# Kernel tuning notes

Hardware: AMD Instinct MI355X
Metric: run time of the kernel (lower is better)

## Reference

```python
import jax, jax.numpy as jnp
import numpy as np

B, T, EMB, H = 8, 1024, 128, 8


def setup_inputs() -> dict:
    key = jax.random.key(0)
    ks = jax.random.split(key, 7)
    s = 0.02
    return {
        "x": jax.random.normal(ks[0], (B, T, EMB), dtype=jnp.float32),
        "mask": jax.random.randint(ks[1], (1, T, T), 0, 2, dtype=jnp.int32),
        "Wk": (jax.random.normal(ks[2], (EMB * H, EMB), dtype=jnp.float32) * s),
        "Wq": (jax.random.normal(ks[3], (EMB * H, EMB), dtype=jnp.float32) * s),
        "Wv": (jax.random.normal(ks[4], (EMB * H, EMB), dtype=jnp.float32) * s),
        "Wu": (jax.random.normal(ks[5], (EMB, EMB * H), dtype=jnp.float32) * s),
        "bu": (jax.random.normal(ks[6], (EMB,), dtype=jnp.float32) * s),
    }


def reference(x, mask, Wk, Wq, Wv, Wu, bu):
    b, t, e = x.shape  # e == emb; per-head dim also == emb in this module
    h = Wk.shape[0] // e
    # projections: (b,t,e) @ (e, h*e) -> (b,t,h,e) -> (b,h,t,e)
    q = (x @ Wq.T).reshape(b, t, h, e).transpose(0, 2, 1, 3)
    k = (x @ Wk.T).reshape(b, t, h, e).transpose(0, 2, 1, 3)
    v = (x @ Wv.T).reshape(b, t, h, e).transpose(0, 2, 1, 3)
    scale = e ** 0.25  # torch scales q and k each by e**(1/4)
    dot = jnp.einsum('bhqe,bhke->bhqk', q / scale, k / scale)
    # causal mask: strictly-upper triangle (offset=1) set to -inf FIRST
    causal = jnp.triu(jnp.ones((t, t), dtype=bool), k=1)
    dot = jnp.where(causal, -jnp.inf, dot)
    # padding mask: where mask==0 set to -1e9 (overwrites -inf where overlapping)
    dot = jnp.where(mask[:, None] == 0, jnp.float32(-1e9), dot)
    attn = jax.nn.softmax(dot, axis=-1)
    out = jnp.einsum('bhqk,bhke->bhqe', attn, v)
    out = out.transpose(0, 2, 1, 3).reshape(b, t, h * e)
    return out @ Wu.T + bu
```

## Files before the change

kernel.cpp:

```cpp
#include <hip/hip_runtime.h>

#define Bn 8
#define Hn 8
#define Tn 1024
#define Dn 128

typedef __attribute__((ext_vector_type(8))) short bf16x8;
typedef __attribute__((ext_vector_type(4))) float f32x4;

typedef __attribute__((address_space(3))) unsigned int lds_as_t;
typedef __attribute__((address_space(1))) const unsigned int glb_as_t;

static __device__ __forceinline__ void gload_lds16(const unsigned short* g, unsigned short* l) {
    __builtin_amdgcn_global_load_lds((glb_as_t*)g, (lds_as_t*)l, 16, 0, 0);
}

static __device__ __forceinline__ unsigned short f2bf(float f) {
    union { float f; unsigned int u; } v; v.f = f;
    unsigned int u = v.u;
    return (unsigned short)((u + 0x7FFFu + ((u >> 16) & 1u)) >> 16);
}

__global__ __launch_bounds__(256) void prep_kernel(
    const float* __restrict__ x,  const float* __restrict__ Wq,
    const float* __restrict__ Wk, const float* __restrict__ Wv,
    const float* __restrict__ Wu, const int* __restrict__ mask,
    unsigned short* __restrict__ xb,  unsigned short* __restrict__ wqB,
    unsigned short* __restrict__ wkB, unsigned short* __restrict__ wvB,
    unsigned short* __restrict__ wuB, unsigned long long* __restrict__ bits)
{
    const int blk = blockIdx.x;
    const int tid = threadIdx.x;

    if (blk < 1408) {
        const float* in; unsigned short* out; int i4;
        if (blk < 1024)      { in = x;  out = xb;  i4 = blk * 256 + tid; }
        else if (blk < 1152) { in = Wq; out = wqB; i4 = (blk - 1024) * 256 + tid; }
        else if (blk < 1280) { in = Wk; out = wkB; i4 = (blk - 1152) * 256 + tid; }
        else                 { in = Wv; out = wvB; i4 = (blk - 1280) * 256 + tid; }
        float4 f = ((const float4*)in)[i4];
        ushort4 o;
        o.x = f2bf(f.x); o.y = f2bf(f.y); o.z = f2bf(f.z); o.w = f2bf(f.w);
        int base = i4 * 4;
        int row = base >> 7, col = base & 127;
        int scol = (((col >> 3) ^ (row & 15)) << 3) | (col & 7);
        *(ushort4*)(out + row * 128 + scol) = o;
    } else if (blk < 1536) {
        int i4 = (blk - 1408) * 256 + tid;
        float4 f = ((const float4*)Wu)[i4];
        ushort4 o;
        o.x = f2bf(f.x); o.y = f2bf(f.y); o.z = f2bf(f.z); o.w = f2bf(f.w);
        ((ushort4*)wuB)[i4] = o;
    } else {
        int wid  = (blk - 1536) * 4 + (tid >> 6);
        int lane = tid & 63;
#pragma unroll
        for (int i = 0; i < 4; i++) {
            int widx = wid * 4 + i;
            int row = widx >> 4, kt = widx & 15;
            int v = mask[row * Tn + kt * 64 + lane];
            unsigned long long b = __ballot(v != 0);
            if (lane == 0) bits[widx] = b;
        }
    }
}

__global__ __launch_bounds__(256, 2) void qkv_kernel(
    const unsigned short* __restrict__ xb,
    const unsigned short* __restrict__ wqB,
    const unsigned short* __restrict__ wkB,
    const unsigned short* __restrict__ wvB,
    unsigned short* __restrict__ Q,
    unsigned short* __restrict__ K,
    unsigned short* __restrict__ Vt)
{
    const int bx = blockIdx.x, by = blockIdx.y;
    const int wave = threadIdx.x >> 6;
    const int lane = threadIdx.x & 63;
    const int l16  = lane & 15;
    const int quad = lane >> 4;
    const int wm = wave & 1, wn = wave >> 1;

    __shared__ __align__(16) unsigned short As[128 * 128];
    __shared__ __align__(16) unsigned short Bs[128 * 128];

    const int which = by >> 3;
    const unsigned short* wsel = (which == 0) ? wqB : (which == 1) ? wkB : wvB;
    const unsigned short* Ag = xb + (size_t)bx * 128 * 128;
    const unsigned short* Bg = wsel + (size_t)(by & 7) * 128 * 128;

#pragma unroll
    for (int i = 0; i < 8; i++) {
        int base = (wave * 8 + i) * 512;
        gload_lds16(Ag + base + lane * 8, &As[base]);
        gload_lds16(Bg + base + lane * 8, &Bs[base]);
    }
    __syncthreads();

    bf16x8 a[4][4];
#pragma unroll
    for (int mt = 0; mt < 4; mt++) {
        int row = wm * 64 + mt * 16 + l16;
#pragma unroll
        for (int ks = 0; ks < 4; ks++)
            a[mt][ks] = *(const bf16x8*)(&As[row * 128 + (((ks * 4 + quad) ^ (row & 15)) << 3)]);
    }

    f32x4 acc[4][4];
#pragma unroll
    for (int nt = 0; nt < 4; nt++) {
        int row = wn * 64 + nt * 16 + l16;
        bf16x8 b4[4];
#pragma unroll
        for (int ks = 0; ks < 4; ks++)
            b4[ks] = *(const bf16x8*)(&Bs[row * 128 + (((ks * 4 + quad) ^ (row & 15)) << 3)]);
#pragma unroll
        for (int mt = 0; mt < 4; mt++) {
            f32x4 c = {0.f, 0.f, 0.f, 0.f};
#pragma unroll
            for (int ks = 0; ks < 4; ks++)
                c = __builtin_amdgcn_mfma_f32_16x16x32_bf16(a[mt][ks], b4[ks], c, 0, 0, 0);
            acc[mt][nt] = c;
        }
    }

    const int h_ = by & 7;
#pragma unroll
    for (int mt = 0; mt < 4; mt++) {
        int m_base = bx * 128 + wm * 64 + mt * 16 + quad * 4;
        int b_ = m_base >> 10;
        int t0 = m_base & 1023;
#pragma unroll
        for (int nt = 0; nt < 4; nt++) {
            int ncol = wn * 64 + nt * 16 + l16;
            if (which == 2) {
                int kt_ = t0 >> 6, tc0 = t0 & 63;
                int e_ = ncol;
                size_t off = ((((size_t)(b_ * Hn + h_) * 16 + kt_) * 128 + e_) << 6)
                           + ((((tc0 >> 3) ^ (e_ & 7)) << 3) | (tc0 & 7));
                ushort4 v4;
                v4.x = f2bf(acc[mt][nt][0]); v4.y = f2bf(acc[mt][nt][1]);
                v4.z = f2bf(acc[mt][nt][2]); v4.w = f2bf(acc[mt][nt][3]);
                *(ushort4*)(Vt + off) = v4;
            } else {
#pragma unroll
                for (int r = 0; r < 4; r++) {
                    int t_ = t0 + r;
                    unsigned short v = f2bf(acc[mt][nt][r]);
                    size_t rowoff = ((size_t)((b_ * Hn + h_) * Tn + t_)) * Dn;
                    if (which == 0) {
                        Q[rowoff + ncol] = v;
                    } else {
                        int nc = ((((ncol >> 3) ^ (t_ & 15)) << 3) | (ncol & 7));
                        K[rowoff + nc] = v;
                    }
                }
            }
        }
    }
}

__global__ __launch_bounds__(256, 2) void attn_kernel(
    const unsigned short* __restrict__ Q,
    const unsigned short* __restrict__ K,
    const unsigned short* __restrict__ Vt,
    const unsigned long long* __restrict__ mbits,
    unsigned short* __restrict__ AO)
{
    const int qt   = 15 - ((blockIdx.x + blockIdx.y) & 15);
    const int bh   = blockIdx.y;
    const int wave = threadIdx.x >> 6;
    const int lane = threadIdx.x & 63;
    const int l16  = lane & 15;
    const int quad = lane >> 4;

    __shared__ __align__(16) unsigned short kbuf[2][64 * 128];
    __shared__ __align__(16) unsigned short vbuf[2][128 * 64];
    __shared__ __align__(16) unsigned short pbuf[4][16][72];

    const unsigned short* Qb = Q  + (size_t)bh * Tn * Dn;
    const unsigned short* Kb = K  + (size_t)bh * Tn * Dn;
    const unsigned short* Vb = Vt + (size_t)bh * (16 * 128 * 64);

    const int q0 = qt * 64 + wave * 16;
    const int qrow = q0 + quad * 4;
    const unsigned long long* mrow = mbits + (size_t)qrow * 16;

    bf16x8 qf[4];
#pragma unroll
    for (int ks = 0; ks < 4; ks++)
        qf[ks] = *(const bf16x8*)(Qb + (size_t)(q0 + l16) * Dn + ks * 32 + quad * 8);

    bf16x8 ones;
#pragma unroll
    for (int j = 0; j < 8; j++) ones[j] = (short)0x3F80;

    f32x4 o[8];
#pragma unroll
    for (int et = 0; et < 8; et++) o[et] = (f32x4){0.f, 0.f, 0.f, 0.f};
    f32x4 lacc = {0.f, 0.f, 0.f, 0.f};

    const float SL = 0.12752041570284543f;

#pragma unroll
    for (int i = 0; i < 4; i++) {
        int base = (wave * 4 + i) * 512;
        gload_lds16(Kb + base + lane * 8, &kbuf[0][base]);
        gload_lds16(Vb + base + lane * 8, &vbuf[0][base]);
    }

    for (int kt = 0; kt <= qt; kt++) {
        const int cur = kt & 1;
        __syncthreads();

        if (kt < qt) {
            const unsigned short* Kg = Kb + (kt + 1) * (64 * 128);
            const unsigned short* Vg = Vb + (kt + 1) * (128 * 64);
#pragma unroll
            for (int i = 0; i < 4; i++) {
                int base = (wave * 4 + i) * 512;
                gload_lds16(Kg + base + lane * 8, &kbuf[cur ^ 1][base]);
                gload_lds16(Vg + base + lane * 8, &vbuf[cur ^ 1][base]);
            }
        }

        unsigned long long mw[4];
#pragma unroll
        for (int r = 0; r < 4; r++) mw[r] = mrow[r * 16 + kt];

        f32x4 s[4];
#pragma unroll
        for (int nt = 0; nt < 4; nt++) {
            bf16x8 b4[4];
#pragma unroll
            for (int ks = 0; ks < 4; ks++)
                b4[ks] = *(const bf16x8*)(&kbuf[cur][(nt * 16 + l16) * 128 + (((ks * 4 + quad) ^ l16) << 3)]);
            f32x4 c = {0.f, 0.f, 0.f, 0.f};
#pragma unroll
            for (int ks = 0; ks < 4; ks++)
                c = __builtin_amdgcn_mfma_f32_16x16x32_bf16(qf[ks], b4[ks], c, 0, 0, 0);
            s[nt] = c;
        }

        const int kc0 = kt * 64;
#pragma unroll
        for (int nt = 0; nt < 4; nt++) {
            int bi = nt * 16 + l16;
            int key = kc0 + bi;
#pragma unroll
            for (int r = 0; r < 4; r++) {
                bool live = ((mw[r] >> bi) & 1ULL) && !(kt == qt && key > qrow + r);
                float p = live ? __builtin_amdgcn_exp2f(s[nt][r] * SL) : 0.f;
                pbuf[wave][quad * 4 + r][bi] = f2bf(p);
            }
        }

        bf16x8 pf[2];
#pragma unroll
        for (int k2 = 0; k2 < 2; k2++)
            pf[k2] = *(const bf16x8*)(&pbuf[wave][l16][k2 * 32 + quad * 8]);

#pragma unroll
        for (int k2 = 0; k2 < 2; k2++)
            lacc = __builtin_amdgcn_mfma_f32_16x16x32_bf16(pf[k2], ones, lacc, 0, 0, 0);
#pragma unroll
        for (int et = 0; et < 8; et++) {
            f32x4 c = o[et];
#pragma unroll
            for (int k2 = 0; k2 < 2; k2++) {
                bf16x8 b = *(const bf16x8*)(&vbuf[cur][(et * 16 + l16) * 64 + (((k2 * 4 + quad) ^ (l16 & 7)) << 3)]);
                c = __builtin_amdgcn_mfma_f32_16x16x32_bf16(pf[k2], b, c, 0, 0, 0);
            }
            o[et] = c;
        }
    }

    {
        bool deg = (lacc[0] == 0.f) | (lacc[1] == 0.f) | (lacc[2] == 0.f) | (lacc[3] == 0.f);
        if (__ballot(deg) != 0ULL) {
            unsigned short dsel[4];
#pragma unroll
            for (int r = 0; r < 4; r++) dsel[r] = (lacc[r] == 0.f) ? (unsigned short)0x3F80 : (unsigned short)0;
            for (int kt = 0; kt < 16; kt++) {
                unsigned long long mw[4];
#pragma unroll
                for (int r = 0; r < 4; r++) mw[r] = mrow[r * 16 + kt];
#pragma unroll
                for (int nt = 0; nt < 4; nt++) {
                    int bi = nt * 16 + l16;
#pragma unroll
                    for (int r = 0; r < 4; r++)
                        pbuf[wave][quad * 4 + r][bi] = ((mw[r] >> bi) & 1ULL) ? (unsigned short)0 : dsel[r];
                }
                bf16x8 pf[2];
#pragma unroll
                for (int k2 = 0; k2 < 2; k2++)
                    pf[k2] = *(const bf16x8*)(&pbuf[wave][l16][k2 * 32 + quad * 8]);
#pragma unroll
                for (int k2 = 0; k2 < 2; k2++)
                    lacc = __builtin_amdgcn_mfma_f32_16x16x32_bf16(pf[k2], ones, lacc, 0, 0, 0);
#pragma unroll
                for (int et = 0; et < 8; et++) {
                    f32x4 c = o[et];
#pragma unroll
                    for (int k2 = 0; k2 < 2; k2++) {
                        const unsigned short* vg = Vb + kt * (128 * 64)
                            + (et * 16 + l16) * 64 + (((k2 * 4 + quad) ^ (l16 & 7)) << 3);
                        bf16x8 b = *(const bf16x8*)vg;
                        c = __builtin_amdgcn_mfma_f32_16x16x32_bf16(pf[k2], b, c, 0, 0, 0);
                    }
                    o[et] = c;
                }
            }
        }
    }

    const int b_ = bh >> 3, h_ = bh & 7;
#pragma unroll
    for (int r = 0; r < 4; r++) {
        float inv = 1.f / lacc[r];
        int q = qrow + r;
        size_t rowoff = (size_t)(b_ * Tn + q) * (Hn * Dn) + h_ * Dn;
#pragma unroll
        for (int et = 0; et < 8; et++)
            AO[rowoff + et * 16 + l16] = f2bf(o[et][r] * inv);
    }
}

__global__ void zero_kernel(float4* __restrict__ p, int n4) {
    int i = blockIdx.x * blockDim.x + threadIdx.x;
    if (i < n4) p[i] = (float4){0.f, 0.f, 0.f, 0.f};
}

__global__ __launch_bounds__(256) void outproj_kernel(
    const unsigned short* __restrict__ AO,
    const unsigned short* __restrict__ wuB,
    const float* __restrict__ bu,
    float* __restrict__ out)
{
    const int wave = threadIdx.x >> 6;
    const int lane = threadIdx.x & 63;
    const int l16  = lane & 15;
    const int quad = lane >> 4;
    const int m0 = blockIdx.x * 64 + wave * 16;
    const int ks0 = blockIdx.y * 16;

    f32x4 acc[8];
#pragma unroll
    for (int nt = 0; nt < 8; nt++) acc[nt] = (f32x4){0.f, 0.f, 0.f, 0.f};

    for (int g = 0; g < 4; g++) {
        int kk = ks0 + g * 4;
        bf16x8 a4[4];
#pragma unroll
        for (int j = 0; j < 4; j++)
            a4[j] = *(const bf16x8*)(AO + (size_t)(m0 + l16) * 1024 + (kk + j) * 32 + quad * 8);
#pragma unroll
        for (int nt = 0; nt < 8; nt++) {
            bf16x8 b4[4];
#pragma unroll
            for (int j = 0; j < 4; j++)
                b4[j] = *(const bf16x8*)(wuB + (size_t)(nt * 16 + l16) * 1024 + (kk + j) * 32 + quad * 8);
#pragma unroll
            for (int j = 0; j < 4; j++)
                acc[nt] = __builtin_amdgcn_mfma_f32_16x16x32_bf16(a4[j], b4[j], acc[nt], 0, 0, 0);
        }
    }

#pragma unroll
    for (int nt = 0; nt < 8; nt++) {
        int n = nt * 16 + l16;
        float bias = (blockIdx.y == 0) ? bu[n] : 0.f;
#pragma unroll
        for (int r = 0; r < 4; r++) {
            int m = m0 + quad * 4 + r;
            atomicAdd(&out[(size_t)m * Dn + n], acc[nt][r] + bias);
        }
    }
}

extern "C" void kernel_launch(void* const* d_in, const int* in_sizes, int n_in,
                              void* d_out, int out_size, void* d_ws, size_t ws_size,
                              hipStream_t stream) {
    const float* x   = (const float*)d_in[0];
    const int* mask  = (const int*)d_in[1];
    const float* Wk  = (const float*)d_in[2];
    const float* Wq  = (const float*)d_in[3];
    const float* Wv  = (const float*)d_in[4];
    const float* Wu  = (const float*)d_in[5];
    const float* bu  = (const float*)d_in[6];
    float* out = (float*)d_out;

    char* ws = (char*)d_ws;
    unsigned short* xb  = (unsigned short*)ws; ws += (size_t)8192 * 128 * 2;
    unsigned short* wqB = (unsigned short*)ws; ws += (size_t)1024 * 128 * 2;
    unsigned short* wkB = (unsigned short*)ws; ws += (size_t)1024 * 128 * 2;
    unsigned short* wvB = (unsigned short*)ws; ws += (size_t)1024 * 128 * 2;
    unsigned short* wuB = (unsigned short*)ws; ws += (size_t)128 * 1024 * 2;
    unsigned short* Qw  = (unsigned short*)ws; ws += (size_t)64 * 1024 * 128 * 2;
    unsigned short* Kw  = (unsigned short*)ws; ws += (size_t)64 * 1024 * 128 * 2;
    unsigned short* Vtw = (unsigned short*)ws; ws += (size_t)64 * 1024 * 128 * 2;
    unsigned short* AOw = (unsigned short*)ws; ws += (size_t)8192 * 1024 * 2;
    unsigned long long* mb = (unsigned long long*)ws; ws += (size_t)1024 * 16 * 8;

    prep_kernel<<<dim3(2560), 256, 0, stream>>>(x, Wq, Wk, Wv, Wu, mask,
                                                xb, wqB, wkB, wvB, wuB, mb);
    zero_kernel<<<dim3(1024), 256, 0, stream>>>((float4*)out, 8192 * 128 / 4);
    qkv_kernel<<<dim3(64, 24), 256, 0, stream>>>(xb, wqB, wkB, wvB, Qw, Kw, Vtw);
    attn_kernel<<<dim3(16, 64), 256, 0, stream>>>(Qw, Kw, Vtw, mb, AOw);
    outproj_kernel<<<dim3(128, 2), 256, 0, stream>>>(AOw, wuB, bu, out);
}
```

Baseline: 179.6 us.

## Read V directly from global in attention, raise occupancy, drop atomic output projection

The attention kernel stops staging V tiles in LDS and loads the V fragments straight from global memory. This halves shared memory use and lets the launch bound request three blocks per CU instead of two. The causal test is simplified to a plain key<=query comparison. The output projection now splits K across the four waves and reduces through shared memory, writing the output once with the bias. That removes the zero-fill kernel and the atomicAdds, at the cost of more global V traffic and latency exposed inside the attention loop.

Result: slower. 184.3 us (+2.6%).

```diff
diff --git a/kernel.cpp b/kernel.cpp
--- a/kernel.cpp
+++ b/kernel.cpp
@@ -160,7 +160,7 @@
     }
 }
 
-__global__ __launch_bounds__(256, 2) void attn_kernel(
+__global__ __launch_bounds__(256, 3) void attn_kernel(
     const unsigned short* __restrict__ Q,
     const unsigned short* __restrict__ K,
     const unsigned short* __restrict__ Vt,
@@ -175,7 +175,6 @@
     const int quad = lane >> 4;
 
     __shared__ __align__(16) unsigned short kbuf[2][64 * 128];
-    __shared__ __align__(16) unsigned short vbuf[2][128 * 64];
     __shared__ __align__(16) unsigned short pbuf[4][16][72];
 
     const unsigned short* Qb = Q  + (size_t)bh * Tn * Dn;
@@ -206,7 +205,6 @@
     for (int i = 0; i < 4; i++) {
         int base = (wave * 4 + i) * 512;
         gload_lds16(Kb + base + lane * 8, &kbuf[0][base]);
-        gload_lds16(Vb + base + lane * 8, &vbuf[0][base]);
     }
 
     for (int kt = 0; kt <= qt; kt++) {
@@ -215,12 +213,10 @@
 
         if (kt < qt) {
             const unsigned short* Kg = Kb + (kt + 1) * (64 * 128);
-            const unsigned short* Vg = Vb + (kt + 1) * (128 * 64);
 #pragma unroll
             for (int i = 0; i < 4; i++) {
                 int base = (wave * 4 + i) * 512;
                 gload_lds16(Kg + base + lane * 8, &kbuf[cur ^ 1][base]);
-                gload_lds16(Vg + base + lane * 8, &vbuf[cur ^ 1][base]);
             }
         }
 
@@ -249,7 +245,7 @@
             int key = kc0 + bi;
 #pragma unroll
             for (int r = 0; r < 4; r++) {
-                bool live = ((mw[r] >> bi) & 1ULL) && !(kt == qt && key > qrow + r);
+                bool live = ((mw[r] >> bi) & 1ULL) && (key <= qrow + r);
                 float p = live ? __builtin_amdgcn_exp2f(s[nt][r] * SL) : 0.f;
                 pbuf[wave][quad * 4 + r][bi] = f2bf(p);
             }
@@ -263,15 +259,14 @@
 #pragma unroll
         for (int k2 = 0; k2 < 2; k2++)
             lacc = __builtin_amdgcn_mfma_f32_16x16x32_bf16(pf[k2], ones, lacc, 0, 0, 0);
+
+        const unsigned short* Vg = Vb + kt * (128 * 64);
 #pragma unroll
         for (int et = 0; et < 8; et++) {
-            f32x4 c = o[et];
-#pragma unroll
-            for (int k2 = 0; k2 < 2; k2++) {
-                bf16x8 b = *(const bf16x8*)(&vbuf[cur][(et * 16 + l16) * 64 + (((k2 * 4 + quad) ^ (l16 & 7)) << 3)]);
-                c = __builtin_amdgcn_mfma_f32_16x16x32_bf16(pf[k2], b, c, 0, 0, 0);
-            }
-            o[et] = c;
+            bf16x8 vb0 = *(const bf16x8*)(Vg + (et * 16 + l16) * 64 + (((0 * 4 + quad) ^ (l16 & 7)) << 3));
+            bf16x8 vb1 = *(const bf16x8*)(Vg + (et * 16 + l16) * 64 + (((1 * 4 + quad) ^ (l16 & 7)) << 3));
+            o[et] = __builtin_amdgcn_mfma_f32_16x16x32_bf16(pf[0], vb0, o[et], 0, 0, 0);
+            o[et] = __builtin_amdgcn_mfma_f32_16x16x32_bf16(pf[1], vb1, o[et], 0, 0, 0);
         }
     }
 
@@ -299,17 +294,14 @@
 #pragma unroll
                 for (int k2 = 0; k2 < 2; k2++)
                     lacc = __builtin_amdgcn_mfma_f32_16x16x32_bf16(pf[k2], ones, lacc, 0, 0, 0);
+                const unsigned short* Vg = Vb + kt * (128 * 64);
 #pragma unroll
                 for (int et = 0; et < 8; et++) {
-                    f32x4 c = o[et];
 #pragma unroll
                     for (int k2 = 0; k2 < 2; k2++) {
-                        const unsigned short* vg = Vb + kt * (128 * 64)
-                            + (et * 16 + l16) * 64 + (((k2 * 4 + quad) ^ (l16 & 7)) << 3);
-                        bf16x8 b = *(const bf16x8*)vg;
-                        c = __builtin_amdgcn_mfma_f32_16x16x32_bf16(pf[k2], b, c, 0, 0, 0);
+                        bf16x8 b = *(const bf16x8*)(Vg + (et * 16 + l16) * 64 + (((k2 * 4 + quad) ^ (l16 & 7)) << 3));
+                        o[et] = __builtin_amdgcn_mfma_f32_16x16x32_bf16(pf[k2], b, o[et], 0, 0, 0);
                     }
-                    o[et] = c;
                 }
             }
         }
@@ -325,11 +317,6 @@
         for (int et = 0; et < 8; et++)
             AO[rowoff + et * 16 + l16] = f2bf(o[et][r] * inv);
     }
-}
-
-__global__ void zero_kernel(float4* __restrict__ p, int n4) {
-    int i = blockIdx.x * blockDim.x + threadIdx.x;
-    if (i < n4) p[i] = (float4){0.f, 0.f, 0.f, 0.f};
 }
 
 __global__ __launch_bounds__(256) void outproj_kernel(
@@ -342,40 +329,52 @@
     const int lane = threadIdx.x & 63;
     const int l16  = lane & 15;
     const int quad = lane >> 4;
-    const int m0 = blockIdx.x * 64 + wave * 16;
-    const int ks0 = blockIdx.y * 16;
-
-    f32x4 acc[8];
-#pragma unroll
-    for (int nt = 0; nt < 8; nt++) acc[nt] = (f32x4){0.f, 0.f, 0.f, 0.f};
-
-    for (int g = 0; g < 4; g++) {
-        int kk = ks0 + g * 4;
-        bf16x8 a4[4];
-#pragma unroll
-        for (int j = 0; j < 4; j++)
-            a4[j] = *(const bf16x8*)(AO + (size_t)(m0 + l16) * 1024 + (kk + j) * 32 + quad * 8);
+    const int m0 = blockIdx.x * 32;
+
+    __shared__ float red[4][32][128];
+
+    f32x4 acc[2][8];
+#pragma unroll
+    for (int ml = 0; ml < 2; ml++)
+#pragma unroll
+        for (int nt = 0; nt < 8; nt++) acc[ml][nt] = (f32x4){0.f, 0.f, 0.f, 0.f};
+
+    const int kk0 = wave * 8;
+#pragma unroll
+    for (int g = 0; g < 8; g++) {
+        int kk = kk0 + g;
+        bf16x8 a0 = *(const bf16x8*)(AO + (size_t)(m0 + l16) * 1024 + kk * 32 + quad * 8);
+        bf16x8 a1 = *(const bf16x8*)(AO + (size_t)(m0 + 16 + l16) * 1024 + kk * 32 + quad * 8);
 #pragma unroll
         for (int nt = 0; nt < 8; nt++) {
-            bf16x8 b4[4];
-#pragma unroll
-            for (int j = 0; j < 4; j++)
-                b4[j] = *(const bf16x8*)(wuB + (size_t)(nt * 16 + l16) * 1024 + (kk + j) * 32 + quad * 8);
-#pragma unroll
-            for (int j = 0; j < 4; j++)
-                acc[nt] = __builtin_amdgcn_mfma_f32_16x16x32_bf16(a4[j], b4[j], acc[nt], 0, 0, 0);
-        }
-    }
-
-#pragma unroll
-    for (int nt = 0; nt < 8; nt++) {
-        int n = nt * 16 + l16;
-        float bias = (blockIdx.y == 0) ? bu[n] : 0.f;
-#pragma unroll
-        for (int r = 0; r < 4; r++) {
-            int m = m0 + quad * 4 + r;
-            atomicAdd(&out[(size_t)m * Dn + n], acc[nt][r] + bias);
-        }
+            bf16x8 b = *(const bf16x8*)(wuB + (size_t)(nt * 16 + l16) * 1024 + kk * 32 + quad * 8);
+            acc[0][nt] = __builtin_amdgcn_mfma_f32_16x16x32_bf16(a0, b, acc[0][nt], 0, 0, 0);
+            acc[1][nt] = __builtin_amdgcn_mfma_f32_16x16x32_bf16(a1, b, acc[1][nt], 0, 0, 0);
+        }
+    }
+
+#pragma unroll
+    for (int ml = 0; ml < 2; ml++)
+#pragma unroll
+        for (int nt = 0; nt < 8; nt++)
+#pragma unroll
+            for (int r = 0; r < 4; r++)
+                red[wave][ml * 16 + quad * 4 + r][nt * 16 + l16] = acc[ml][nt][r];
+    __syncthreads();
+
+#pragma unroll
+    for (int i = 0; i < 4; i++) {
+        int flat4 = i * 256 + threadIdx.x;
+        int row = flat4 >> 5, c4 = (flat4 & 31) * 4;
+        f32x4 v = *(const f32x4*)(&red[0][row][c4]);
+#pragma unroll
+        for (int w = 1; w < 4; w++) {
+            f32x4 p = *(const f32x4*)(&red[w][row][c4]);
+            v[0] += p[0]; v[1] += p[1]; v[2] += p[2]; v[3] += p[3];
+        }
+        float4 bb = *(const float4*)(bu + c4);
+        v[0] += bb.x; v[1] += bb.y; v[2] += bb.z; v[3] += bb.w;
+        *(f32x4*)(out + (size_t)(m0 + row) * Dn + c4) = v;
     }
 }
 
@@ -405,8 +404,7 @@
 
     prep_kernel<<<dim3(2560), 256, 0, stream>>>(x, Wq, Wk, Wv, Wu, mask,
                                                 xb, wqB, wkB, wvB, wuB, mb);
-    zero_kernel<<<dim3(1024), 256, 0, stream>>>((float4*)out, 8192 * 128 / 4);
     qkv_kernel<<<dim3(64, 24), 256, 0, stream>>>(xb, wqB, wkB, wvB, Qw, Kw, Vtw);
     attn_kernel<<<dim3(16, 64), 256, 0, stream>>>(Qw, Kw, Vtw, mb, AOw);
-    outproj_kernel<<<dim3(128, 2), 256, 0, stream>>>(AOw, wuB, bu, out);
-}
+    outproj_kernel<<<dim3(256), 256, 0, stream>>>(AOw, wuB, bu, out);
+}
```
